# Kernel tuning notes

Hardware: AMD Instinct MI355X
Metric: run time of the kernel (lower is better)

## Reference

```python
import jax, jax.numpy as jnp
import numpy as np

TAU = 2.0
ALPHA = 4.0  # spikingjelly surrogate.Sigmoid default
NUM_HEADS = 8


def lif(x, v_th):
    # Multi-step LIF over leading time axis T. v_reset=0, hard reset, tau=2.
    # Forward: Heaviside spike; backward: sigmoid surrogate via straight-through.
    def step(v, xt):
        v = v + (xt - v) / TAU
        hard = (v >= v_th).astype(xt.dtype)
        soft = jax.nn.sigmoid(ALPHA * (v - v_th))
        spike = soft + jax.lax.stop_gradient(hard - soft)
        v = v * (1.0 - jax.lax.stop_gradient(hard))  # detach_reset hard reset to 0
        return v, spike
    _, out = jax.lax.scan(step, jnp.zeros_like(x[0]), x)
    return out


def conv_bn_lif(x, w, scale, bias, v_th=1.0):
    # 1x1 conv (no bias) + folded eval-mode BatchNorm + LIF.
    # x: [T,B,C,H,W], w: [Cout,Cin], scale/bias: [Cout]
    y = jnp.einsum('tbchw,dc->tbdhw', x, w)
    y = y * scale[:, None, None] + bias[:, None, None]
    return lif(y, v_th)


def setup_inputs() -> dict:
    key = jax.random.key(0)
    ks = jax.random.split(key, 14)
    T, B, C, H, W = 4, 32, 384, 14, 14
    x = jax.random.normal(ks[0], (T, B, C, H, W), dtype=jnp.float32)
    def conv_params(k):
        k1, k2, k3 = jax.random.split(k, 3)
        w = jax.random.normal(k1, (C, C), dtype=jnp.float32) * (1.0 / np.sqrt(C))
        scale = jax.random.uniform(k2, (C,), dtype=jnp.float32, minval=0.5, maxval=1.5)
        bias = jax.random.normal(k3, (C,), dtype=jnp.float32) * 0.1
        return w, scale, bias
    wq, sq, bq = conv_params(ks[1])
    wk, sk, bk = conv_params(ks[2])
    wv, sv, bv = conv_params(ks[3])
    wp, sp, bp = conv_params(ks[4])
    return {"x": x, "wq": wq, "sq": sq, "bq": bq, "wk": wk, "sk": sk, "bk": bk,
            "wv": wv, "sv": sv, "bv": bv, "wp": wp, "sp": sp, "bp": bp}


def reference(x, wq, sq, bq, wk, sk, bk, wv, sv, bv, wp, sp, bp):
    T, B, C, H, W = x.shape
    h = NUM_HEADS
    d = C // h
    N = H * W
    # QKV: conv+BN+LIF -> binary spikes [T,B,C,H,W]
    qs = conv_bn_lif(x, wq, sq, bq)
    ks_ = conv_bn_lif(x, wk, sk, bk)
    vs = conv_bn_lif(x, wv, sv, bv)
    # [T,B,C,H,W] -> [T,B,h,d,N] -> [T,B,h,N,d]
    def to_heads(t):
        return t.reshape(T, B, h, d, N).transpose(0, 1, 2, 4, 3)
    q, k, v = to_heads(qs), to_heads(ks_), to_heads(vs)
    attn = jnp.einsum('tbhnd,tbhmd->tbhnm', q, k)
    out = jnp.einsum('tbhnm,tbhmd->tbhnd', attn, v) * 0.125
    out = lif(out, 0.5)  # attn_lif v_threshold=0.5
    # [T,B,h,N,d] -> [T,B,h,d,N] -> [T,B,C,H,W]
    out = out.transpose(0, 1, 2, 4, 3).reshape(T, B, C, H, W)
    out = conv_bn_lif(out, wp, sp, bp)
    return out
```

## Files before the change

kernel.cpp:

```cpp
#include <hip/hip_runtime.h>


#define T_ 4
#define B_ 32
#define C_ 384
#define N_ 196
#define NH_ 8
#define D_ 48
#define TB_ (T_ * B_)
#define CN_ ((size_t)C_ * N_)
#define BCN4_ (B_ * C_ * (N_ / 4))
#define TBCN_ ((size_t)T_ * B_ * C_ * N_)
typedef unsigned long long u64;

__global__ __launch_bounds__(256, 2) void gemm_f32(
    const float* __restrict__ X, const float* __restrict__ W0,
    const float* __restrict__ W1, const float* __restrict__ W2,
    float* __restrict__ P)
{
  const int g = blockIdx.z;
  const float* __restrict__ W = (g == 0) ? W0 : (g == 1) ? W1 : W2;
  const int co0 = blockIdx.y * 128;
  const int j0 = blockIdx.x * 128;
  __shared__ float As[16][128];
  __shared__ float Bs[16][128];
  const int tid = threadIdx.x;
  const int tx = tid & 15, ty = tid >> 4;

  const int bcol = (tid & 31) * 4;
  const int bk = tid >> 5;
  const int bj = j0 + bcol;
  const int btb = bj / N_;
  const float* xb = X + (size_t)btb * CN_ + (bj - btb * N_);
  const int arow = tid >> 1;
  const int ac8 = (tid & 1) * 8;

  float acc[8][8] = {};
  for (int c0 = 0; c0 < C_; c0 += 16) {
    const float* wrow = W + (size_t)(co0 + arow) * C_ + c0 + ac8;
    const float4 a0 = *(const float4*)wrow;
    const float4 a1 = *(const float4*)(wrow + 4);
    As[ac8 + 0][arow] = a0.x; As[ac8 + 1][arow] = a0.y;
    As[ac8 + 2][arow] = a0.z; As[ac8 + 3][arow] = a0.w;
    As[ac8 + 4][arow] = a1.x; As[ac8 + 5][arow] = a1.y;
    As[ac8 + 6][arow] = a1.z; As[ac8 + 7][arow] = a1.w;
    *(float4*)&Bs[bk][bcol]     = *(const float4*)(xb + (size_t)(c0 + bk) * N_);
    *(float4*)&Bs[bk + 8][bcol] = *(const float4*)(xb + (size_t)(c0 + bk + 8) * N_);
    __syncthreads();
#pragma unroll
    for (int k = 0; k < 16; ++k) {
      float a[8], b[8];
      *(float4*)&a[0] = *(const float4*)&As[k][ty * 4];
      *(float4*)&a[4] = *(const float4*)&As[k][64 + ty * 4];
      *(float4*)&b[0] = *(const float4*)&Bs[k][tx * 4];
      *(float4*)&b[4] = *(const float4*)&Bs[k][64 + tx * 4];
#pragma unroll
      for (int i = 0; i < 8; ++i)
#pragma unroll
        for (int j = 0; j < 8; ++j)
          acc[i][j] = fmaf(a[i], b[j], acc[i][j]);
    }
    __syncthreads();
  }
#pragma unroll
  for (int cg = 0; cg < 2; ++cg) {
    const int jj = j0 + cg * 64 + tx * 4;
    const int tb = jj / N_;
    float* pb = P + (size_t)(g * TB_ + tb) * CN_ + (jj - tb * N_);
#pragma unroll
    for (int rg = 0; rg < 2; ++rg) {
#pragma unroll
      for (int i = 0; i < 4; ++i) {
        const int r = rg * 4 + i;
        const int co = co0 + rg * 64 + ty * 4 + i;
        *(float4*)&pb[(size_t)co * N_] = make_float4(
            acc[r][cg * 4 + 0], acc[r][cg * 4 + 1],
            acc[r][cg * 4 + 2], acc[r][cg * 4 + 3]);
      }
    }
  }
}

__global__ __launch_bounds__(256) void lif4(
    const float* __restrict__ In, float* __restrict__ Out,
    const float* __restrict__ s0, const float* __restrict__ b0, float vth)
{
  const long u = (long)blockIdx.x * 256 + threadIdx.x;
  if (u >= BCN4_) return;
  const long r = u;
  const int c = (int)((r / (N_ / 4)) % C_);
  const bool has_bn = (s0 != nullptr);
  const float sc = has_bn ? s0[c] : 1.0f;
  const float bi = has_bn ? b0[c] : 0.0f;
  const float4* In4 = (const float4*)In;
  float4* Out4 = (float4*)Out;
  float v[4] = {0.f, 0.f, 0.f, 0.f};
#pragma unroll
  for (int t = 0; t < T_; ++t) {
    const long idx = (long)t * BCN4_ + r;
    const float4 y4 = In4[idx];
    float y[4] = {y4.x, y4.y, y4.z, y4.w};
    float o[4];
#pragma unroll
    for (int e = 0; e < 4; ++e) {
      const float yb = has_bn ? __fadd_rn(__fmul_rn(y[e], sc), bi) : y[e];
      v[e] = __fadd_rn(v[e], __fmul_rn(__fsub_rn(yb, v[e]), 0.5f));
      const bool fire = (v[e] >= vth);
      o[e] = fire ? 1.0f : 0.0f;
      v[e] = fire ? 0.0f : v[e];
    }
    Out4[idx] = make_float4(o[0], o[1], o[2], o[3]);
  }
}

__global__ __launch_bounds__(256) void k_mask(
    const float* __restrict__ P, u64* __restrict__ MSK,
    const float* __restrict__ sq, const float* __restrict__ bq,
    const float* __restrict__ sk, const float* __restrict__ bk,
    const float* __restrict__ sv, const float* __restrict__ bv)
{
  const int wave = threadIdx.x >> 6, lane = threadIdx.x & 63;
  const int task = blockIdx.x * 4 + wave;
  const int j = task % D_;
  int r = task / D_;
  const int b = r & 31; r >>= 5;
  const int h = r & 7;  r >>= 3;
  const int g = r;
  const int c = h * D_ + j;
  const float sc = (g == 0 ? sq : g == 1 ? sk : sv)[c];
  const float bi = (g == 0 ? bq : g == 1 ? bk : bv)[c];
  const float* base = P + (size_t)g * TB_ * CN_ + (size_t)b * CN_ + (size_t)c * N_;

  float y[4][T_];
  bool act[4];
#pragma unroll
  for (int w = 0; w < 4; ++w) {
    const int m = w * 64 + lane;
    act[w] = (m < N_);
    const int mc = act[w] ? m : (N_ - 1);
#pragma unroll
    for (int t = 0; t < T_; ++t)
      y[w][t] = base[(size_t)t * B_ * CN_ + mc];
  }
  u64* mb = MSK + ((size_t)(h * 32 + b) * 3 + g) * (T_ * D_ * 4) + j * 4;
  float v[4] = {0.f, 0.f, 0.f, 0.f};
#pragma unroll
  for (int t = 0; t < T_; ++t) {
#pragma unroll
    for (int w = 0; w < 4; ++w) {
      const float yb = __fadd_rn(__fmul_rn(y[w][t], sc), bi);
      v[w] = __fadd_rn(v[w], __fmul_rn(__fsub_rn(yb, v[w]), 0.5f));
      const bool fire = (v[w] >= 1.0f);
      if (fire) v[w] = 0.f;
      const u64 bl = __ballot(fire && act[w]);
      if (lane == 0) mb[(size_t)t * (D_ * 4) + w] = bl;
    }
  }
}

__global__ __launch_bounds__(1024) void k_attn(
    const u64* __restrict__ MSK, float* __restrict__ O)
{
  const int h = blockIdx.x;
  const int b = blockIdx.y;
  __shared__ u64 msk[3][T_][D_][4];
  __shared__ u64 qT[T_][208];
  __shared__ u64 Gp[T_][8][D_];
  const int tid = threadIdx.x;
  const int wave = tid >> 6, lane = tid & 63;

  {
    const u64* ms = MSK + (size_t)(h * 32 + b) * 2304;
    u64* mf = &msk[0][0][0][0];
    for (int off = tid; off < 2304; off += 1024) mf[off] = ms[off];
  }
  __syncthreads();

  {
    const int t = wave >> 2, w = wave & 3;
    const int n = w * 64 + lane;
    u64 qr = 0ull;
#pragma unroll 8
    for (int j = 0; j < D_; ++j)
      qr |= ((msk[0][t][j][w] >> lane) & 1ull) << j;
    if (n < N_) qT[t][n] = qr;
  }
  for (int task = wave; task < T_ * D_; task += 16) {
    const int t = task / D_, d = task - (task / D_) * D_;
    const bool ja = (lane < D_);
    const int j = ja ? lane : (D_ - 1);
    const u64* kj = msk[1][t][j];
    const u64* vd = msk[2][t][d];
    const int gi = __popcll(kj[0] & vd[0]) + __popcll(kj[1] & vd[1]) +
                   __popcll(kj[2] & vd[2]) + __popcll(kj[3] & vd[3]);
#pragma unroll
    for (int p = 0; p < 8; ++p) {
      const u64 bl = __ballot(ja && ((gi >> p) & 1));
      if (lane == 0) Gp[t][p][d] = bl;
    }
  }
  __syncthreads();

  const int u = tid;
  if (u < 4 * N_) {
    const int dq = u / N_;
    const int n = u - dq * N_;
    const int d0 = dq * 12;
    float vmem[12];
#pragma unroll
    for (int i = 0; i < 12; ++i) vmem[i] = 0.f;
    for (int t = 0; t < T_; ++t) {
      const u64 qr = qT[t][n];
      float* ob = O + ((size_t)(t * B_ + b) * C_ + h * D_ + d0) * N_ + n;
#pragma unroll
      for (int i = 0; i < 12; ++i) {
        int acc = 0;
#pragma unroll
        for (int p = 0; p < 8; ++p)
          acc += __popcll(qr & Gp[t][p][d0 + i]) << p;
        const float y = __int2float_rn(acc) * 0.125f;
        vmem[i] = __fadd_rn(vmem[i], __fmul_rn(__fsub_rn(y, vmem[i]), 0.5f));
        const bool fire = (vmem[i] >= 0.5f);
        ob[(size_t)i * N_] = fire ? 1.0f : 0.0f;
        if (fire) vmem[i] = 0.f;
      }
    }
  }
}

extern "C" void kernel_launch(void* const* d_in, const int* in_sizes, int n_in,
                              void* d_out, int out_size, void* d_ws, size_t ws_size,
                              hipStream_t stream) {
  const float* x  = (const float*)d_in[0];
  const float* wq = (const float*)d_in[1];
  const float* sq = (const float*)d_in[2];
  const float* bq = (const float*)d_in[3];
  const float* wk = (const float*)d_in[4];
  const float* sk = (const float*)d_in[5];
  const float* bk = (const float*)d_in[6];
  const float* wv = (const float*)d_in[7];
  const float* sv = (const float*)d_in[8];
  const float* bv = (const float*)d_in[9];
  const float* wp = (const float*)d_in[10];
  const float* sp = (const float*)d_in[11];
  const float* bp = (const float*)d_in[12];
  float* out = (float*)d_out;

  float* P = (float*)d_ws;
  float* O = P + 3 * TBCN_;
  u64* MSK = (u64*)(P + 4 * TBCN_);
  float* P2 = P;

  gemm_f32<<<dim3(196, 3, 3), 256, 0, stream>>>(x, wq, wk, wv, P);
  k_mask<<<dim3(9216), 256, 0, stream>>>(P, MSK, sq, bq, sk, bk, sv, bv);
  k_attn<<<dim3(NH_, B_), 1024, 0, stream>>>(MSK, O);
  gemm_f32<<<dim3(196, 3, 1), 256, 0, stream>>>(O, wp, wp, wp, P2);
  lif4<<<dim3((BCN4_ + 255) / 256), 256, 0, stream>>>(P2, out, sp, bp, 1.0f);
}
```

Baseline: 505.9 us.

## Prefetch GEMM tiles into registers, vectorize mask loads, split attention blocks

The GEMM now loads the next K-slice of W and X into registers while computing the current tile, so global-load latency overlaps the FMA work. k_mask switches to float4 loads with a per-lane 4-column interleaved bit layout, and k_attn decodes that layout. k_attn is split into four 256-thread blocks per (head, batch), one per group of output channels. This raises block count and occupancy but recomputes the Gram bitmasks and transposed Q in each block.

```diff
diff --git a/kernel.cpp b/kernel.cpp
--- a/kernel.cpp
+++ b/kernel.cpp
@@ -34,19 +34,29 @@
   const float* xb = X + (size_t)btb * CN_ + (bj - btb * N_);
   const int arow = tid >> 1;
   const int ac8 = (tid & 1) * 8;
+  const float* wrow0 = W + (size_t)(co0 + arow) * C_ + ac8;
+
+  float4 pa0 = *(const float4*)(wrow0);
+  float4 pa1 = *(const float4*)(wrow0 + 4);
+  float4 pb0 = *(const float4*)(xb + (size_t)bk * N_);
+  float4 pb1 = *(const float4*)(xb + (size_t)(bk + 8) * N_);
 
   float acc[8][8] = {};
   for (int c0 = 0; c0 < C_; c0 += 16) {
-    const float* wrow = W + (size_t)(co0 + arow) * C_ + c0 + ac8;
-    const float4 a0 = *(const float4*)wrow;
-    const float4 a1 = *(const float4*)(wrow + 4);
-    As[ac8 + 0][arow] = a0.x; As[ac8 + 1][arow] = a0.y;
-    As[ac8 + 2][arow] = a0.z; As[ac8 + 3][arow] = a0.w;
-    As[ac8 + 4][arow] = a1.x; As[ac8 + 5][arow] = a1.y;
-    As[ac8 + 6][arow] = a1.z; As[ac8 + 7][arow] = a1.w;
-    *(float4*)&Bs[bk][bcol]     = *(const float4*)(xb + (size_t)(c0 + bk) * N_);
-    *(float4*)&Bs[bk + 8][bcol] = *(const float4*)(xb + (size_t)(c0 + bk + 8) * N_);
     __syncthreads();
+    As[ac8 + 0][arow] = pa0.x; As[ac8 + 1][arow] = pa0.y;
+    As[ac8 + 2][arow] = pa0.z; As[ac8 + 3][arow] = pa0.w;
+    As[ac8 + 4][arow] = pa1.x; As[ac8 + 5][arow] = pa1.y;
+    As[ac8 + 6][arow] = pa1.z; As[ac8 + 7][arow] = pa1.w;
+    *(float4*)&Bs[bk][bcol] = pb0;
+    *(float4*)&Bs[bk + 8][bcol] = pb1;
+    __syncthreads();
+    if (c0 + 16 < C_) {
+      pa0 = *(const float4*)(wrow0 + c0 + 16);
+      pa1 = *(const float4*)(wrow0 + c0 + 20);
+      pb0 = *(const float4*)(xb + (size_t)(c0 + 16 + bk) * N_);
+      pb1 = *(const float4*)(xb + (size_t)(c0 + 24 + bk) * N_);
+    }
 #pragma unroll
     for (int k = 0; k < 16; ++k) {
       float a[8], b[8];
@@ -60,7 +70,6 @@
         for (int j = 0; j < 8; ++j)
           acc[i][j] = fmaf(a[i], b[j], acc[i][j]);
     }
-    __syncthreads();
   }
 #pragma unroll
   for (int cg = 0; cg < 2; ++cg) {
@@ -129,42 +138,38 @@
   const int c = h * D_ + j;
   const float sc = (g == 0 ? sq : g == 1 ? sk : sv)[c];
   const float bi = (g == 0 ? bq : g == 1 ? bk : bv)[c];
-  const float* base = P + (size_t)g * TB_ * CN_ + (size_t)b * CN_ + (size_t)c * N_;
-
-  float y[4][T_];
-  bool act[4];
-#pragma unroll
-  for (int w = 0; w < 4; ++w) {
-    const int m = w * 64 + lane;
-    act[w] = (m < N_);
-    const int mc = act[w] ? m : (N_ - 1);
-#pragma unroll
-    for (int t = 0; t < T_; ++t)
-      y[w][t] = base[(size_t)t * B_ * CN_ + mc];
-  }
+  const bool act = (lane < 49);
+  const int nq = act ? lane * 4 : 192;
+  const float* base = P + (size_t)g * TB_ * CN_ + (size_t)b * CN_
+                        + (size_t)c * N_ + nq;
+  float4 y[T_];
+#pragma unroll
+  for (int t = 0; t < T_; ++t)
+    y[t] = *(const float4*)(base + (size_t)t * B_ * CN_);
+
   u64* mb = MSK + ((size_t)(h * 32 + b) * 3 + g) * (T_ * D_ * 4) + j * 4;
   float v[4] = {0.f, 0.f, 0.f, 0.f};
 #pragma unroll
   for (int t = 0; t < T_; ++t) {
-#pragma unroll
-    for (int w = 0; w < 4; ++w) {
-      const float yb = __fadd_rn(__fmul_rn(y[w][t], sc), bi);
-      v[w] = __fadd_rn(v[w], __fmul_rn(__fsub_rn(yb, v[w]), 0.5f));
-      const bool fire = (v[w] >= 1.0f);
-      if (fire) v[w] = 0.f;
-      const u64 bl = __ballot(fire && act[w]);
-      if (lane == 0) mb[(size_t)t * (D_ * 4) + w] = bl;
-    }
-  }
-}
-
-__global__ __launch_bounds__(1024) void k_attn(
+    const float ya[4] = {y[t].x, y[t].y, y[t].z, y[t].w};
+#pragma unroll
+    for (int e = 0; e < 4; ++e) {
+      const float yb = __fadd_rn(__fmul_rn(ya[e], sc), bi);
+      v[e] = __fadd_rn(v[e], __fmul_rn(__fsub_rn(yb, v[e]), 0.5f));
+      const bool fire = (v[e] >= 1.0f);
+      if (fire) v[e] = 0.f;
+      const u64 bl = __ballot(fire && act);
+      if (lane == 0) mb[(size_t)t * (D_ * 4) + e] = bl;
+    }
+  }
+}
+
+__global__ __launch_bounds__(256) void k_attn(
     const u64* __restrict__ MSK, float* __restrict__ O)
 {
-  const int h = blockIdx.x;
-  const int b = blockIdx.y;
+  const int h = blockIdx.x, b = blockIdx.y, dq = blockIdx.z;
   __shared__ u64 msk[3][T_][D_][4];
-  __shared__ u64 qT[T_][208];
+  __shared__ u64 qT[T_][200];
   __shared__ u64 Gp[T_][8][D_];
   const int tid = threadIdx.x;
   const int wave = tid >> 6, lane = tid & 63;
@@ -172,20 +177,20 @@
   {
     const u64* ms = MSK + (size_t)(h * 32 + b) * 2304;
     u64* mf = &msk[0][0][0][0];
-    for (int off = tid; off < 2304; off += 1024) mf[off] = ms[off];
+    for (int off = tid; off < 2304; off += 256) mf[off] = ms[off];
   }
   __syncthreads();
 
-  {
-    const int t = wave >> 2, w = wave & 3;
-    const int n = w * 64 + lane;
+  for (int u = tid; u < T_ * N_; u += 256) {
+    const int t = u / N_, n = u - (u / N_) * N_;
+    const int w = n & 3, s = n >> 2;
     u64 qr = 0ull;
 #pragma unroll 8
     for (int j = 0; j < D_; ++j)
-      qr |= ((msk[0][t][j][w] >> lane) & 1ull) << j;
-    if (n < N_) qT[t][n] = qr;
-  }
-  for (int task = wave; task < T_ * D_; task += 16) {
+      qr |= ((msk[0][t][j][w] >> s) & 1ull) << j;
+    qT[t][n] = qr;
+  }
+  for (int task = wave; task < T_ * D_; task += 4) {
     const int t = task / D_, d = task - (task / D_) * D_;
     const bool ja = (lane < D_);
     const int j = ja ? lane : (D_ - 1);
@@ -201,10 +206,8 @@
   }
   __syncthreads();
 
-  const int u = tid;
-  if (u < 4 * N_) {
-    const int dq = u / N_;
-    const int n = u - dq * N_;
+  if (tid < N_) {
+    const int n = tid;
     const int d0 = dq * 12;
     float vmem[12];
 #pragma unroll
@@ -253,7 +256,7 @@
 
   gemm_f32<<<dim3(196, 3, 3), 256, 0, stream>>>(x, wq, wk, wv, P);
   k_mask<<<dim3(9216), 256, 0, stream>>>(P, MSK, sq, bq, sk, bk, sv, bv);
-  k_attn<<<dim3(NH_, B_), 1024, 0, stream>>>(MSK, O);
+  k_attn<<<dim3(NH_, B_, 4), 256, 0, stream>>>(MSK, O);
   gemm_f32<<<dim3(196, 3, 1), 256, 0, stream>>>(O, wp, wp, wp, P2);
   lif4<<<dim3((BCN4_ + 255) / 256), 256, 0, stream>>>(P2, out, sp, bp, 1.0f);
 }
```

Measured after the change: 526.7 us. +4.1%, slower.

## Double K-tile with register prefetch in GEMM; vectorize Gp reads in attention

Applied to the files above, without the earlier changes.

The FP32 GEMM now stages a 32-deep K tile instead of 16 and loads the next tile's W and X values into registers while the current tile is computed. This hides global-memory latency and halves the number of barrier pairs. In exchange it doubles shared memory per block and adds registers, which can lower occupancy under launch_bounds(256,2). The attention kernel also reads the Gp bit-planes as 128-bit ulonglong2 loads and accumulates all 12 outputs before running the LIF, cutting the number of LDS instructions.

```diff
diff --git a/kernel.cpp b/kernel.cpp
--- a/kernel.cpp
+++ b/kernel.cpp
@@ -22,8 +22,8 @@
   const float* __restrict__ W = (g == 0) ? W0 : (g == 1) ? W1 : W2;
   const int co0 = blockIdx.y * 128;
   const int j0 = blockIdx.x * 128;
-  __shared__ float As[16][128];
-  __shared__ float Bs[16][128];
+  __shared__ float As[32][128];
+  __shared__ float Bs[32][128];
   const int tid = threadIdx.x;
   const int tx = tid & 15, ty = tid >> 4;
 
@@ -33,22 +33,37 @@
   const int btb = bj / N_;
   const float* xb = X + (size_t)btb * CN_ + (bj - btb * N_);
   const int arow = tid >> 1;
-  const int ac8 = (tid & 1) * 8;
+  const int ac16 = (tid & 1) * 16;
+  const float* wrow0 = W + (size_t)(co0 + arow) * C_ + ac16;
+
+  float4 pa[4], pb[4];
+#pragma unroll
+  for (int q = 0; q < 4; ++q) {
+    pa[q] = *(const float4*)(wrow0 + q * 4);
+    pb[q] = *(const float4*)(xb + (size_t)(bk + 8 * q) * N_);
+  }
 
   float acc[8][8] = {};
-  for (int c0 = 0; c0 < C_; c0 += 16) {
-    const float* wrow = W + (size_t)(co0 + arow) * C_ + c0 + ac8;
-    const float4 a0 = *(const float4*)wrow;
-    const float4 a1 = *(const float4*)(wrow + 4);
-    As[ac8 + 0][arow] = a0.x; As[ac8 + 1][arow] = a0.y;
-    As[ac8 + 2][arow] = a0.z; As[ac8 + 3][arow] = a0.w;
-    As[ac8 + 4][arow] = a1.x; As[ac8 + 5][arow] = a1.y;
-    As[ac8 + 6][arow] = a1.z; As[ac8 + 7][arow] = a1.w;
-    *(float4*)&Bs[bk][bcol]     = *(const float4*)(xb + (size_t)(c0 + bk) * N_);
-    *(float4*)&Bs[bk + 8][bcol] = *(const float4*)(xb + (size_t)(c0 + bk + 8) * N_);
+  for (int c0 = 0; c0 < C_; c0 += 32) {
     __syncthreads();
 #pragma unroll
-    for (int k = 0; k < 16; ++k) {
+    for (int q = 0; q < 4; ++q) {
+      As[ac16 + q * 4 + 0][arow] = pa[q].x;
+      As[ac16 + q * 4 + 1][arow] = pa[q].y;
+      As[ac16 + q * 4 + 2][arow] = pa[q].z;
+      As[ac16 + q * 4 + 3][arow] = pa[q].w;
+      *(float4*)&Bs[bk + 8 * q][bcol] = pb[q];
+    }
+    __syncthreads();
+    if (c0 + 32 < C_) {
+#pragma unroll
+      for (int q = 0; q < 4; ++q) {
+        pa[q] = *(const float4*)(wrow0 + c0 + 32 + q * 4);
+        pb[q] = *(const float4*)(xb + (size_t)(c0 + 32 + bk + 8 * q) * N_);
+      }
+    }
+#pragma unroll
+    for (int k = 0; k < 32; ++k) {
       float a[8], b[8];
       *(float4*)&a[0] = *(const float4*)&As[k][ty * 4];
       *(float4*)&a[4] = *(const float4*)&As[k][64 + ty * 4];
@@ -60,20 +75,19 @@
         for (int j = 0; j < 8; ++j)
           acc[i][j] = fmaf(a[i], b[j], acc[i][j]);
     }
-    __syncthreads();
   }
 #pragma unroll
   for (int cg = 0; cg < 2; ++cg) {
     const int jj = j0 + cg * 64 + tx * 4;
     const int tb = jj / N_;
-    float* pb = P + (size_t)(g * TB_ + tb) * CN_ + (jj - tb * N_);
+    float* pb2 = P + (size_t)(g * TB_ + tb) * CN_ + (jj - tb * N_);
 #pragma unroll
     for (int rg = 0; rg < 2; ++rg) {
 #pragma unroll
       for (int i = 0; i < 4; ++i) {
         const int r = rg * 4 + i;
         const int co = co0 + rg * 64 + ty * 4 + i;
-        *(float4*)&pb[(size_t)co * N_] = make_float4(
+        *(float4*)&pb2[(size_t)co * N_] = make_float4(
             acc[r][cg * 4 + 0], acc[r][cg * 4 + 1],
             acc[r][cg * 4 + 2], acc[r][cg * 4 + 3]);
       }
@@ -211,14 +225,23 @@
     for (int i = 0; i < 12; ++i) vmem[i] = 0.f;
     for (int t = 0; t < T_; ++t) {
       const u64 qr = qT[t][n];
+      int acc[12];
+#pragma unroll
+      for (int i = 0; i < 12; ++i) acc[i] = 0;
+#pragma unroll
+      for (int p = 0; p < 8; ++p) {
+        const ulonglong2* gp = (const ulonglong2*)&Gp[t][p][d0];
+#pragma unroll
+        for (int ii = 0; ii < 6; ++ii) {
+          const ulonglong2 gv = gp[ii];
+          acc[2 * ii + 0] += __popcll(qr & gv.x) << p;
+          acc[2 * ii + 1] += __popcll(qr & gv.y) << p;
+        }
+      }
       float* ob = O + ((size_t)(t * B_ + b) * C_ + h * D_ + d0) * N_ + n;
 #pragma unroll
       for (int i = 0; i < 12; ++i) {
-        int acc = 0;
-#pragma unroll
-        for (int p = 0; p < 8; ++p)
-          acc += __popcll(qr & Gp[t][p][d0 + i]) << p;
-        const float y = __int2float_rn(acc) * 0.125f;
+        const float y = __int2float_rn(acc[i]) * 0.125f;
         vmem[i] = __fadd_rn(vmem[i], __fmul_rn(__fsub_rn(y, vmem[i]), 0.5f));
         const bool fire = (vmem[i] >= 0.5f);
         ob[(size_t)i * N_] = fire ? 1.0f : 0.0f;
```

After: 589.3 us. 1.16x slower.

## Double-buffer GEMM tiles with direct global-to-LDS loads and register prefetch

Applied to the files above, without the earlier changes.

Rewrites the fp32 GEMM main loop to double-buffer the A and B shared-memory tiles, so the next k-slice loads while the current one is computed, and uses one barrier per iteration instead of two. The X tile is loaded with the global_load_lds builtin, which writes straight into LDS and skips the trip through registers. The weight rows are prefetched into registers two iterations ahead. This doubles LDS use and drops the 2-blocks-per-CU launch bound hint, which may change occupancy and register allocation.

```diff
diff --git a/kernel.cpp b/kernel.cpp
--- a/kernel.cpp
+++ b/kernel.cpp
@@ -13,7 +13,7 @@
 #define TBCN_ ((size_t)T_ * B_ * C_ * N_)
 typedef unsigned long long u64;
 
-__global__ __launch_bounds__(256, 2) void gemm_f32(
+__global__ __launch_bounds__(256) void gemm_f32(
     const float* __restrict__ X, const float* __restrict__ W0,
     const float* __restrict__ W1, const float* __restrict__ W2,
     float* __restrict__ P)
@@ -22,43 +22,73 @@
   const float* __restrict__ W = (g == 0) ? W0 : (g == 1) ? W1 : W2;
   const int co0 = blockIdx.y * 128;
   const int j0 = blockIdx.x * 128;
-  __shared__ float As[16][128];
-  __shared__ float Bs[16][128];
+  __shared__ float As[2][16][128];
+  __shared__ float Bs[2][16][128];
   const int tid = threadIdx.x;
   const int tx = tid & 15, ty = tid >> 4;
-
-  const int bcol = (tid & 31) * 4;
-  const int bk = tid >> 5;
-  const int bj = j0 + bcol;
+  const int wv = tid >> 6, lane = tid & 63;
+  const int krow = lane >> 5;
+
+  const int bj = j0 + (lane & 31) * 4;
   const int btb = bj / N_;
-  const float* xb = X + (size_t)btb * CN_ + (bj - btb * N_);
+  const float* xcol = X + (size_t)btb * CN_ + (bj - btb * N_);
+  const float* src0 = xcol + (size_t)(4 * wv + krow) * N_;
+  const float* src1 = src0 + 2 * N_;
+
   const int arow = tid >> 1;
   const int ac8 = (tid & 1) * 8;
+  const float* wrow0 = W + (size_t)(co0 + arow) * C_ + ac8;
+
+  __builtin_amdgcn_global_load_lds(
+      (const __attribute__((address_space(1))) void*)src0,
+      (__attribute__((address_space(3))) void*)&Bs[0][4 * wv][0], 16, 0, 0);
+  __builtin_amdgcn_global_load_lds(
+      (const __attribute__((address_space(1))) void*)src1,
+      (__attribute__((address_space(3))) void*)&Bs[0][4 * wv + 2][0], 16, 0, 0);
+  float4 a0 = *(const float4*)(wrow0);
+  float4 a1 = *(const float4*)(wrow0 + 4);
+  As[0][ac8 + 0][arow] = a0.x; As[0][ac8 + 1][arow] = a0.y;
+  As[0][ac8 + 2][arow] = a0.z; As[0][ac8 + 3][arow] = a0.w;
+  As[0][ac8 + 4][arow] = a1.x; As[0][ac8 + 5][arow] = a1.y;
+  As[0][ac8 + 6][arow] = a1.z; As[0][ac8 + 7][arow] = a1.w;
+  float4 n0 = *(const float4*)(wrow0 + 16);
+  float4 n1 = *(const float4*)(wrow0 + 20);
+  __syncthreads();
 
   float acc[8][8] = {};
-  for (int c0 = 0; c0 < C_; c0 += 16) {
-    const float* wrow = W + (size_t)(co0 + arow) * C_ + c0 + ac8;
-    const float4 a0 = *(const float4*)wrow;
-    const float4 a1 = *(const float4*)(wrow + 4);
-    As[ac8 + 0][arow] = a0.x; As[ac8 + 1][arow] = a0.y;
-    As[ac8 + 2][arow] = a0.z; As[ac8 + 3][arow] = a0.w;
-    As[ac8 + 4][arow] = a1.x; As[ac8 + 5][arow] = a1.y;
-    As[ac8 + 6][arow] = a1.z; As[ac8 + 7][arow] = a1.w;
-    *(float4*)&Bs[bk][bcol]     = *(const float4*)(xb + (size_t)(c0 + bk) * N_);
-    *(float4*)&Bs[bk + 8][bcol] = *(const float4*)(xb + (size_t)(c0 + bk + 8) * N_);
-    __syncthreads();
+  for (int i = 0; i < 24; ++i) {
+    const int cur = i & 1, nxt = cur ^ 1;
+    if (i < 23) {
+      const float* s0 = src0 + (size_t)(i + 1) * 16 * N_;
+      const float* s1 = s0 + 2 * N_;
+      __builtin_amdgcn_global_load_lds(
+          (const __attribute__((address_space(1))) void*)s0,
+          (__attribute__((address_space(3))) void*)&Bs[nxt][4 * wv][0], 16, 0, 0);
+      __builtin_amdgcn_global_load_lds(
+          (const __attribute__((address_space(1))) void*)s1,
+          (__attribute__((address_space(3))) void*)&Bs[nxt][4 * wv + 2][0], 16, 0, 0);
+      As[nxt][ac8 + 0][arow] = n0.x; As[nxt][ac8 + 1][arow] = n0.y;
+      As[nxt][ac8 + 2][arow] = n0.z; As[nxt][ac8 + 3][arow] = n0.w;
+      As[nxt][ac8 + 4][arow] = n1.x; As[nxt][ac8 + 5][arow] = n1.y;
+      As[nxt][ac8 + 6][arow] = n1.z; As[nxt][ac8 + 7][arow] = n1.w;
+      if (i < 22) {
+        const float* wn = wrow0 + (i + 2) * 16;
+        n0 = *(const float4*)(wn);
+        n1 = *(const float4*)(wn + 4);
+      }
+    }
 #pragma unroll
     for (int k = 0; k < 16; ++k) {
       float a[8], b[8];
-      *(float4*)&a[0] = *(const float4*)&As[k][ty * 4];
-      *(float4*)&a[4] = *(const float4*)&As[k][64 + ty * 4];
-      *(float4*)&b[0] = *(const float4*)&Bs[k][tx * 4];
-      *(float4*)&b[4] = *(const float4*)&Bs[k][64 + tx * 4];
-#pragma unroll
-      for (int i = 0; i < 8; ++i)
-#pragma unroll
-        for (int j = 0; j < 8; ++j)
-          acc[i][j] = fmaf(a[i], b[j], acc[i][j]);
+      *(float4*)&a[0] = *(const float4*)&As[cur][k][ty * 4];
+      *(float4*)&a[4] = *(const float4*)&As[cur][k][64 + ty * 4];
+      *(float4*)&b[0] = *(const float4*)&Bs[cur][k][tx * 4];
+      *(float4*)&b[4] = *(const float4*)&Bs[cur][k][64 + tx * 4];
+#pragma unroll
+      for (int ii = 0; ii < 8; ++ii)
+#pragma unroll
+        for (int jj = 0; jj < 8; ++jj)
+          acc[ii][jj] = fmaf(a[ii], b[jj], acc[ii][jj]);
     }
     __syncthreads();
   }
```

Result: no change. 508.5 us (+0.5%).
